# Kernel tuning notes

Hardware: AMD Instinct MI355X
Metric: run time of the kernel (lower is better)

## Reference

```python
import jax, jax.numpy as jnp
import numpy as np

N_NODES = 50000
N_EDGES = 300000
D = 256  # node/edge feature dim; MLP input = 3*D = 768


def setup_inputs() -> dict:
    key = jax.random.key(0)
    ks = jax.random.split(key, 5)
    x_node = jax.random.normal(ks[0], (N_NODES, D), dtype=jnp.float32)
    x_edge = jax.random.normal(ks[1], (N_EDGES, D), dtype=jnp.float32)
    edge_index = jax.random.randint(ks[2], (2, N_EDGES), 0, N_NODES, dtype=jnp.int64)
    # MLP params: Linear(3*D, D) -> ReLU -> Linear(D, D)
    W1 = jax.random.normal(ks[3], (3 * D, D), dtype=jnp.float32) * (1.0 / np.sqrt(3 * D))
    b1 = jnp.zeros((D,), dtype=jnp.float32)
    W2 = jax.random.normal(ks[4], (D, D), dtype=jnp.float32) * (1.0 / np.sqrt(D))
    b2 = jnp.zeros((D,), dtype=jnp.float32)
    return {"x_node": x_node, "x_edge": x_edge, "edge_index": edge_index,
            "W1": W1, "b1": b1, "W2": W2, "b2": b2}


def reference(x_node, x_edge, edge_index, W1, b1, W2, b2):
    # gather src/dst node feats and concat with edge feats: [E, 3*D]
    src = x_node[edge_index[0]]
    dst = x_node[edge_index[1]]
    h = jnp.concatenate([src, dst, x_edge], axis=1)
    # MLP (custom_func): Linear -> ReLU -> Linear
    h = jax.nn.relu(h @ W1 + b1)
    x_edge_ = h @ W2 + b2
    return x_edge_
```

## Files before the change

### kernel.cpp

```cpp
#include <hip/hip_runtime.h>


typedef __attribute__((ext_vector_type(8))) short short8;
typedef __attribute__((ext_vector_type(4))) float f32x4;

typedef __attribute__((address_space(1))) unsigned int* gp1_t;
typedef __attribute__((address_space(3))) unsigned int* lp3_t;

#define AS_OFF 0
#define BS_OFF 8192
#define HS_OFF 40960
#define SMEM_SZ 73728
#define LDO 260

__device__ __forceinline__ unsigned short f2b(float f) {
  unsigned int u = __float_as_uint(f);
  return (unsigned short)((u + 0x7FFFu + ((u >> 16) & 1u)) >> 16);
}
__device__ __forceinline__ unsigned int f2b2(float lo, float hi) {
  return (unsigned int)f2b(lo) | ((unsigned int)f2b(hi) << 16);
}
__device__ __forceinline__ void gload16(const void* g, void* l) {
  __builtin_amdgcn_global_load_lds((gp1_t)g, (lp3_t)l, 16, 0, 0);
}

__global__ void prep_w_kernel(const float* __restrict__ w,
                              unsigned short* __restrict__ wp, int total) {
  int i = blockIdx.x * 256 + threadIdx.x;
  if (i >= total) return;
  int kc = i >> 13;
  int rem = i & 8191;
  int n = rem >> 5;
  int kin = rem & 31;
  wp[i] = f2b(w[(size_t)(kc * 32 + kin) * 256 + n]);
}

__global__ void conv_bf16_kernel(const float* __restrict__ x,
                                 unsigned short* __restrict__ y, int n4) {
  int i = blockIdx.x * 256 + threadIdx.x;
  if (i >= n4) return;
  float4 v = ((const float4*)x)[i];
  ushort4 u;
  u.x = f2b(v.x); u.y = f2b(v.y); u.z = f2b(v.z); u.w = f2b(v.w);
  ((ushort4*)y)[i] = u;
}

__global__ __launch_bounds__(256, 2) void edge_mlp_kernel(
    const float* __restrict__ xnode, const float* __restrict__ xedge,
    const int* __restrict__ eidx,
    const unsigned short* __restrict__ nodeb, int use_nodeb,
    const unsigned short* __restrict__ wt1p, const float* __restrict__ b1,
    const unsigned short* __restrict__ wt2p, const float* __restrict__ b2,
    float* __restrict__ out, int E) {
  __shared__ __align__(16) char smem[SMEM_SZ];
  char* As = smem + AS_OFF;
  char* Bs = smem + BS_OFF;
  char* Hs = smem + HS_OFF;

  const int t = threadIdx.x;
  const int w = t >> 6, l = t & 63;
  const int lr = l & 15, lk = l >> 4;
  const int row4 = t >> 2;
  const int c4 = t & 3;

  const int ebase = blockIdx.x * 64;
  int e = ebase + row4;
  if (e >= E) e = E - 1;
  const int isrc = eidx[e], idst = eidx[E + e];

  f32x4 acc[4][4];
#pragma unroll
  for (int i = 0; i < 4; ++i)
#pragma unroll
    for (int j = 0; j < 4; ++j) acc[i][j] = (f32x4)0.0f;

  auto stageB = [&](const unsigned short* wp, int kc, int buf) {
    const char* g = (const char*)wp + (size_t)kc * 16384 + t * 16;
    char* lb = Bs + buf * 16384 + (w << 10);
#pragma unroll
    for (int q = 0; q < 4; ++q) gload16(g + q * 4096, lb + q * 4096);
  };
  auto stageA_node = [&](int kc, int buf) {
    const int node = (kc < 8) ? isrc : idst;
    const char* g = (const char*)nodeb + (size_t)node * 512 + (kc & 7) * 64 + c4 * 16;
    gload16(g, As + buf * 4096 + (w << 10));
  };
  auto stageA_load = [&](int kc, float4& m0, float4& m1) {
    const float* src;
    if (kc < 8)        src = xnode + (size_t)isrc * 256 + kc * 32 + c4 * 8;
    else if (kc < 16)  src = xnode + (size_t)idst * 256 + (kc - 8) * 32 + c4 * 8;
    else               src = xedge + (size_t)e * 256 + (kc - 16) * 32 + c4 * 8;
    m0 = *(const float4*)src;
    m1 = *(const float4*)(src + 4);
  };
  auto stageA_write = [&](int buf, float4 m0, float4 m1) {
    uint4 u;
    u.x = f2b2(m0.x, m0.y); u.y = f2b2(m0.z, m0.w);
    u.z = f2b2(m1.x, m1.y); u.w = f2b2(m1.z, m1.w);
    *(uint4*)(As + buf * 4096 + t * 16) = u;
  };

  auto compute1 = [&](int buf) {
    short8 af[4], bf[4];
    const char* ab = As + buf * 4096;
    const char* bb = Bs + buf * 16384;
#pragma unroll
    for (int mi = 0; mi < 4; ++mi)
      af[mi] = *(const short8*)(ab + (mi * 16 + lr) * 64 + lk * 16);
#pragma unroll
    for (int ni = 0; ni < 4; ++ni)
      bf[ni] = *(const short8*)(bb + (w * 64 + ni * 16 + lr) * 64 + lk * 16);
#pragma unroll
    for (int mi = 0; mi < 4; ++mi)
#pragma unroll
      for (int ni = 0; ni < 4; ++ni)
        acc[mi][ni] = __builtin_amdgcn_mfma_f32_16x16x32_bf16(
            af[mi], bf[ni], acc[mi][ni], 0, 0, 0);
  };

  stageB(wt1p, 0, 0);
  if (use_nodeb) {
    stageA_node(0, 0);
  } else {
    float4 a0, a1;
    stageA_load(0, a0, a1);
    stageA_write(0, a0, a1);
  }
  __syncthreads();

  for (int kc = 0; kc < 24; ++kc) {
    const int cur = kc & 1, nb = cur ^ 1;
    float4 m0, m1;
    bool man = false;
    if (kc < 23) {
      const int nk = kc + 1;
      stageB(wt1p, nk, nb);
      if (use_nodeb && nk < 16) {
        stageA_node(nk, nb);
      } else {
        stageA_load(nk, m0, m1);
        man = true;
      }
    } else {
      stageB(wt2p, 0, nb);
    }
    compute1(cur);
    if (man) stageA_write(nb, m0, m1);
    __syncthreads();
  }

#pragma unroll
  for (int ni = 0; ni < 4; ++ni) {
    const int col = w * 64 + ni * 16 + lr;
    const float bias = b1[col];
    const int cole = col & ~1;
    const int chunk = cole >> 3;
    const int cb = (cole & 6) * 2;
#pragma unroll
    for (int mi = 0; mi < 4; ++mi) {
      float v[4], p[4];
#pragma unroll
      for (int r = 0; r < 4; ++r) {
        float x = acc[mi][ni][r] + bias;
        v[r] = x > 0.f ? x : 0.f;
        acc[mi][ni][r] = 0.f;
      }
#pragma unroll
      for (int r = 0; r < 4; ++r) p[r] = __shfl_xor(v[r], 1, 64);
      const int r0 = (lr & 1) ? 2 : 0;
#pragma unroll
      for (int rr = 0; rr < 2; ++rr) {
        const int r = r0 + rr;
        const int row = mi * 16 + lk * 4 + r;
        const float lo = (lr & 1) ? p[r] : v[r];
        const float hi = (lr & 1) ? v[r] : p[r];
        *(unsigned int*)(Hs + row * 512 + ((chunk ^ (row & 7)) << 4) + cb) = f2b2(lo, hi);
      }
    }
  }
  __syncthreads();

  for (int kc2 = 0; kc2 < 8; ++kc2) {
    const int cur = kc2 & 1, nb = cur ^ 1;
    if (kc2 < 7) stageB(wt2p, kc2 + 1, nb);
    {
      short8 af[4], bf[4];
      const char* bb = Bs + cur * 16384;
#pragma unroll
      for (int mi = 0; mi < 4; ++mi) {
        const int row = mi * 16 + lr;
        af[mi] = *(const short8*)(Hs + row * 512 + (((kc2 * 4 + lk) ^ (row & 7)) << 4));
      }
#pragma unroll
      for (int ni = 0; ni < 4; ++ni)
        bf[ni] = *(const short8*)(bb + (w * 64 + ni * 16 + lr) * 64 + lk * 16);
#pragma unroll
      for (int mi = 0; mi < 4; ++mi)
#pragma unroll
        for (int ni = 0; ni < 4; ++ni)
          acc[mi][ni] = __builtin_amdgcn_mfma_f32_16x16x32_bf16(
              af[mi], bf[ni], acc[mi][ni], 0, 0, 0);
    }
    __syncthreads();
  }

  float* outst = (float*)smem;
#pragma unroll
  for (int ni = 0; ni < 4; ++ni) {
    const int col = w * 64 + ni * 16 + lr;
    const float bias = b2[col];
#pragma unroll
    for (int mi = 0; mi < 4; ++mi)
#pragma unroll
      for (int r = 0; r < 4; ++r)
        outst[(mi * 16 + lk * 4 + r) * LDO + col] = acc[mi][ni][r] + bias;
  }
  __syncthreads();
#pragma unroll
  for (int it = 0; it < 16; ++it) {
    const int idx = it * 1024 + t * 4;
    const int lrow = idx >> 8;
    const int cc = idx & 255;
    const int grow = ebase + lrow;
    if (grow < E)
      *(float4*)(out + (size_t)grow * 256 + cc) =
          *(const float4*)(outst + lrow * LDO + cc);
  }
}

extern "C" void kernel_launch(void* const* d_in, const int* in_sizes, int n_in,
                              void* d_out, int out_size, void* d_ws, size_t ws_size,
                              hipStream_t stream) {
  const float* xnode = (const float*)d_in[0];
  const float* xedge = (const float*)d_in[1];
  const int* eidx = (const int*)d_in[2];
  const float* W1 = (const float*)d_in[3];
  const float* b1 = (const float*)d_in[4];
  const float* W2 = (const float*)d_in[5];
  const float* b2 = (const float*)d_in[6];
  float* out = (float*)d_out;

  const int NN = in_sizes[0] / 256;
  const int E = in_sizes[1] / 256;

  char* ws = (char*)d_ws;
  unsigned short* wt1p = (unsigned short*)ws;
  unsigned short* wt2p = (unsigned short*)(ws + 24 * 16384);
  unsigned short* nodeb = (unsigned short*)(ws + 32 * 16384);
  const size_t need = (size_t)32 * 16384 + (size_t)NN * 512;
  const int use_nodeb = (ws_size >= need) ? 1 : 0;

  prep_w_kernel<<<(24 * 8192 + 255) / 256, 256, 0, stream>>>(W1, wt1p, 24 * 8192);
  prep_w_kernel<<<(8 * 8192 + 255) / 256, 256, 0, stream>>>(W2, wt2p, 8 * 8192);
  if (use_nodeb) {
    const int n4 = NN * 64;
    conv_bf16_kernel<<<(n4 + 255) / 256, 256, 0, stream>>>(xnode, nodeb, n4);
  }

  edge_mlp_kernel<<<(E + 63) / 64, 256, 0, stream>>>(
      xnode, xedge, eidx, nodeb, use_nodeb, wt1p, b1, wt2p, b2, out, E);
}
```

Before: 379.8 us.

## Enlarge edge tile to 256 rows with 512-thread blocks and swizzled LDS layout

The fused edge MLP kernel now processes 256 edges per block with 8 waves (2x4 wave grid, 128x64 per wave). It uses K-steps of 64, XOR-swizzled A/B tiles in 128 KB of LDS, and a reordered weight prepack that matches the swizzle. The second GEMM reads W2 fragments straight from global memory into registers with double buffering instead of staging them in LDS. The output is written back in four 64-row passes. The aim is more weight reuse per block and fewer LDS bank conflicts, at the cost of one block per CU and higher register pressure from 32 accumulators per thread.

Result: faster. 372.0 us (-2.1%).

```diff
diff --git a/kernel.cpp b/kernel.cpp
--- a/kernel.cpp
+++ b/kernel.cpp
@@ -3,14 +3,10 @@
 
 typedef __attribute__((ext_vector_type(8))) short short8;
 typedef __attribute__((ext_vector_type(4))) float f32x4;
-
 typedef __attribute__((address_space(1))) unsigned int* gp1_t;
 typedef __attribute__((address_space(3))) unsigned int* lp3_t;
 
-#define AS_OFF 0
-#define BS_OFF 8192
-#define HS_OFF 40960
-#define SMEM_SZ 73728
+#define SMEM_SZ 131072
 #define LDO 260
 
 __device__ __forceinline__ unsigned short f2b(float f) {
@@ -28,11 +24,13 @@
                               unsigned short* __restrict__ wp, int total) {
   int i = blockIdx.x * 256 + threadIdx.x;
   if (i >= total) return;
-  int kc = i >> 13;
-  int rem = i & 8191;
-  int n = rem >> 5;
-  int kin = rem & 31;
-  wp[i] = f2b(w[(size_t)(kc * 32 + kin) * 256 + n]);
+  int step = i >> 14;
+  int rem = i & 16383;
+  int n = rem >> 6;
+  int s = (rem >> 3) & 7;
+  int j = i & 7;
+  int k = step * 64 + (((s ^ (n & 7)) << 3) | j);
+  wp[i] = f2b(w[(size_t)k * 256 + n]);
 }
 
 __global__ void conv_bf16_kernel(const float* __restrict__ x,
@@ -45,7 +43,7 @@
   ((ushort4*)y)[i] = u;
 }
 
-__global__ __launch_bounds__(256, 2) void edge_mlp_kernel(
+__global__ __launch_bounds__(512) void edge_mlp_full(
     const float* __restrict__ xnode, const float* __restrict__ xedge,
     const int* __restrict__ eidx,
     const unsigned short* __restrict__ nodeb, int use_nodeb,
@@ -53,111 +51,125 @@
     const unsigned short* __restrict__ wt2p, const float* __restrict__ b2,
     float* __restrict__ out, int E) {
   __shared__ __align__(16) char smem[SMEM_SZ];
-  char* As = smem + AS_OFF;
-  char* Bs = smem + BS_OFF;
-  char* Hs = smem + HS_OFF;
-
-  const int t = threadIdx.x;
-  const int w = t >> 6, l = t & 63;
+
+  const int t = threadIdx.x, w = t >> 6, l = t & 63;
   const int lr = l & 15, lk = l >> 4;
-  const int row4 = t >> 2;
-  const int c4 = t & 3;
-
-  const int ebase = blockIdx.x * 64;
-  int e = ebase + row4;
-  if (e >= E) e = E - 1;
-  const int isrc = eidx[e], idst = eidx[E + e];
-
-  f32x4 acc[4][4];
-#pragma unroll
-  for (int i = 0; i < 4; ++i)
+  const int wr = w >> 2, wc = w & 3;
+  const int ebase = blockIdx.x * 256;
+
+  int nsrcq[4], ndstq[4];
+#pragma unroll
+  for (int q = 0; q < 4; ++q) {
+    int rq = 32 * w + 8 * q + (l >> 3);
+    int eq = ebase + rq;
+    if (eq >= E) eq = E - 1;
+    nsrcq[q] = eidx[eq];
+    ndstq[q] = eidx[E + eq];
+  }
+  const int swz16 = ((l & 7) ^ ((l >> 3) & 7)) << 4;
+  const int r2 = t >> 1;
+  int e2 = ebase + r2;
+  if (e2 >= E) e2 = E - 1;
+  const int ns2 = eidx[e2], nd2 = eidx[E + e2];
+
+  f32x4 acc[8][4];
+#pragma unroll
+  for (int i = 0; i < 8; ++i)
 #pragma unroll
     for (int j = 0; j < 4; ++j) acc[i][j] = (f32x4)0.0f;
 
-  auto stageB = [&](const unsigned short* wp, int kc, int buf) {
-    const char* g = (const char*)wp + (size_t)kc * 16384 + t * 16;
-    char* lb = Bs + buf * 16384 + (w << 10);
-#pragma unroll
-    for (int q = 0; q < 4; ++q) gload16(g + q * 4096, lb + q * 4096);
-  };
-  auto stageA_node = [&](int kc, int buf) {
-    const int node = (kc < 8) ? isrc : idst;
-    const char* g = (const char*)nodeb + (size_t)node * 512 + (kc & 7) * 64 + c4 * 16;
-    gload16(g, As + buf * 4096 + (w << 10));
-  };
-  auto stageA_load = [&](int kc, float4& m0, float4& m1) {
-    const float* src;
-    if (kc < 8)        src = xnode + (size_t)isrc * 256 + kc * 32 + c4 * 8;
-    else if (kc < 16)  src = xnode + (size_t)idst * 256 + (kc - 8) * 32 + c4 * 8;
-    else               src = xedge + (size_t)e * 256 + (kc - 16) * 32 + c4 * 8;
-    m0 = *(const float4*)src;
-    m1 = *(const float4*)(src + 4);
-  };
-  auto stageA_write = [&](int buf, float4 m0, float4 m1) {
-    uint4 u;
-    u.x = f2b2(m0.x, m0.y); u.y = f2b2(m0.z, m0.w);
-    u.z = f2b2(m1.x, m1.y); u.w = f2b2(m1.z, m1.w);
-    *(uint4*)(As + buf * 4096 + t * 16) = u;
-  };
-
-  auto compute1 = [&](int buf) {
-    short8 af[4], bf[4];
-    const char* ab = As + buf * 4096;
-    const char* bb = Bs + buf * 16384;
-#pragma unroll
-    for (int mi = 0; mi < 4; ++mi)
-      af[mi] = *(const short8*)(ab + (mi * 16 + lr) * 64 + lk * 16);
-#pragma unroll
-    for (int ni = 0; ni < 4; ++ni)
-      bf[ni] = *(const short8*)(bb + (w * 64 + ni * 16 + lr) * 64 + lk * 16);
-#pragma unroll
-    for (int mi = 0; mi < 4; ++mi)
-#pragma unroll
-      for (int ni = 0; ni < 4; ++ni)
-        acc[mi][ni] = __builtin_amdgcn_mfma_f32_16x16x32_bf16(
-            af[mi], bf[ni], acc[mi][ni], 0, 0, 0);
-  };
-
-  stageB(wt1p, 0, 0);
-  if (use_nodeb) {
-    stageA_node(0, 0);
-  } else {
-    float4 a0, a1;
-    stageA_load(0, a0, a1);
-    stageA_write(0, a0, a1);
-  }
+  auto stageB = [&](int step, int buf) {
+    const char* g = (const char*)wt1p + (size_t)step * 32768 + (t << 4);
+    char* d = smem + 65536 + buf * 32768 + (w << 10) + (l << 4);
+#pragma unroll
+    for (int q = 0; q < 4; ++q) gload16(g + q * 8192, d + q * 8192);
+  };
+  auto stageA_node = [&](int s, int buf) {
+    const int colb = (s & 3) * 128;
+    char* d = smem + buf * 32768 + (w << 12) + (l << 4);
+#pragma unroll
+    for (int q = 0; q < 4; ++q) {
+      const int nid = (s < 4) ? nsrcq[q] : ndstq[q];
+      gload16((const char*)nodeb + (size_t)nid * 512 + colb + swz16,
+              d + (q << 10));
+    }
+  };
+  auto stageA_f32 = [&](const float* base, int rowid, int coloff, int buf) {
+    const int rb = r2 & 7;
+    float4 v[8];
+#pragma unroll
+    for (int jj = 0; jj < 4; ++jj) {
+      const int j = (t & 1) * 4 + jj;
+      const float* p = base + (size_t)rowid * 256 + coloff + j * 8;
+      v[2 * jj] = ((const float4*)p)[0];
+      v[2 * jj + 1] = ((const float4*)p)[1];
+    }
+#pragma unroll
+    for (int jj = 0; jj < 4; ++jj) {
+      const int j = (t & 1) * 4 + jj;
+      uint4 u;
+      u.x = f2b2(v[2 * jj].x, v[2 * jj].y);
+      u.y = f2b2(v[2 * jj].z, v[2 * jj].w);
+      u.z = f2b2(v[2 * jj + 1].x, v[2 * jj + 1].y);
+      u.w = f2b2(v[2 * jj + 1].z, v[2 * jj + 1].w);
+      *(uint4*)(smem + buf * 32768 + r2 * 128 + ((j ^ rb) << 4)) = u;
+    }
+  };
+  auto stageA = [&](int s, int buf) {
+    if (s < 8) {
+      if (use_nodeb) stageA_node(s, buf);
+      else stageA_f32(xnode, (s < 4) ? ns2 : nd2, (s & 3) * 64, buf);
+    } else {
+      stageA_f32(xedge, e2, (s - 8) * 64, buf);
+    }
+  };
+  auto compute = [&](int k) {
+    const char* A = smem + (k & 1) * 32768;
+    const char* B = smem + 65536 + (k & 1) * 32768;
+    __builtin_amdgcn_s_setprio(1);
+#pragma unroll
+    for (int ks = 0; ks < 2; ++ks) {
+      short8 bf[4];
+#pragma unroll
+      for (int ni = 0; ni < 4; ++ni) {
+        const int n = wc * 64 + ni * 16 + lr;
+        bf[ni] = *(const short8*)(B + n * 128 + (((ks * 4 + lk) ^ (n & 7)) << 4));
+      }
+#pragma unroll
+      for (int mi = 0; mi < 8; ++mi) {
+        const int m = wr * 128 + mi * 16 + lr;
+        short8 af = *(const short8*)(A + m * 128 + (((ks * 4 + lk) ^ (m & 7)) << 4));
+#pragma unroll
+        for (int ni = 0; ni < 4; ++ni)
+          acc[mi][ni] = __builtin_amdgcn_mfma_f32_16x16x32_bf16(
+              af, bf[ni], acc[mi][ni], 0, 0, 0);
+      }
+    }
+    __builtin_amdgcn_s_setprio(0);
+  };
+
+  stageA(0, 0);
+  stageB(0, 0);
   __syncthreads();
-
-  for (int kc = 0; kc < 24; ++kc) {
-    const int cur = kc & 1, nb = cur ^ 1;
-    float4 m0, m1;
-    bool man = false;
-    if (kc < 23) {
-      const int nk = kc + 1;
-      stageB(wt1p, nk, nb);
-      if (use_nodeb && nk < 16) {
-        stageA_node(nk, nb);
-      } else {
-        stageA_load(nk, m0, m1);
-        man = true;
-      }
-    } else {
-      stageB(wt2p, 0, nb);
-    }
-    compute1(cur);
-    if (man) stageA_write(nb, m0, m1);
+  for (int k = 0; k < 12; ++k) {
+    if (k + 1 < 12) {
+      stageB(k + 1, (k + 1) & 1);
+      stageA(k + 1, (k + 1) & 1);
+    }
+    compute(k);
     __syncthreads();
   }
 
+  char* Hs = smem;
 #pragma unroll
   for (int ni = 0; ni < 4; ++ni) {
-    const int col = w * 64 + ni * 16 + lr;
+    const int col = wc * 64 + ni * 16 + lr;
     const float bias = b1[col];
     const int cole = col & ~1;
     const int chunk = cole >> 3;
     const int cb = (cole & 6) * 2;
 #pragma unroll
-    for (int mi = 0; mi < 4; ++mi) {
+    for (int mi = 0; mi < 8; ++mi) {
       float v[4], p[4];
 #pragma unroll
       for (int r = 0; r < 4; ++r) {
@@ -171,60 +183,78 @@
 #pragma unroll
       for (int rr = 0; rr < 2; ++rr) {
         const int r = r0 + rr;
-        const int row = mi * 16 + lk * 4 + r;
+        const int row = wr * 128 + mi * 16 + lk * 4 + r;
         const float lo = (lr & 1) ? p[r] : v[r];
         const float hi = (lr & 1) ? v[r] : p[r];
-        *(unsigned int*)(Hs + row * 512 + ((chunk ^ (row & 7)) << 4) + cb) = f2b2(lo, hi);
+        *(unsigned int*)(Hs + row * 512 + ((chunk ^ (row & 7)) << 4) + cb) =
+            f2b2(lo, hi);
       }
     }
   }
   __syncthreads();
 
-  for (int kc2 = 0; kc2 < 8; ++kc2) {
-    const int cur = kc2 & 1, nb = cur ^ 1;
-    if (kc2 < 7) stageB(wt2p, kc2 + 1, nb);
-    {
-      short8 af[4], bf[4];
-      const char* bb = Bs + cur * 16384;
-#pragma unroll
-      for (int mi = 0; mi < 4; ++mi) {
-        const int row = mi * 16 + lr;
-        af[mi] = *(const short8*)(Hs + row * 512 + (((kc2 * 4 + lk) ^ (row & 7)) << 4));
-      }
+  short8 bfA[4], bfB[4];
+  auto loadB2 = [&](int pair, short8 (&bf)[4]) {
+    const char* wb = (const char*)wt2p + (pair >> 1) * 32768;
+    const int ksl = (pair & 1) * 4 + lk;
+#pragma unroll
+    for (int ni = 0; ni < 4; ++ni) {
+      const int n = wc * 64 + ni * 16 + lr;
+      bf[ni] = *(const short8*)(wb + n * 128 + ((ksl ^ (n & 7)) << 4));
+    }
+  };
+  auto mfmaH = [&](int pair, short8 (&bf)[4]) {
+    const int j = (pair >> 1) * 8 + (pair & 1) * 4 + lk;
+    __builtin_amdgcn_s_setprio(1);
+#pragma unroll
+    for (int mi = 0; mi < 8; ++mi) {
+      const int m = wr * 128 + mi * 16 + lr;
+      short8 af = *(const short8*)(Hs + m * 512 + ((j ^ (m & 7)) << 4));
 #pragma unroll
       for (int ni = 0; ni < 4; ++ni)
-        bf[ni] = *(const short8*)(bb + (w * 64 + ni * 16 + lr) * 64 + lk * 16);
-#pragma unroll
-      for (int mi = 0; mi < 4; ++mi)
-#pragma unroll
-        for (int ni = 0; ni < 4; ++ni)
-          acc[mi][ni] = __builtin_amdgcn_mfma_f32_16x16x32_bf16(
-              af[mi], bf[ni], acc[mi][ni], 0, 0, 0);
-    }
+        acc[mi][ni] = __builtin_amdgcn_mfma_f32_16x16x32_bf16(
+            af, bf[ni], acc[mi][ni], 0, 0, 0);
+    }
+    __builtin_amdgcn_s_setprio(0);
+  };
+  loadB2(0, bfA);
+#pragma unroll
+  for (int pair = 0; pair < 8; pair += 2) {
+    if (pair + 1 < 8) loadB2(pair + 1, bfB);
+    mfmaH(pair, bfA);
+    if (pair + 2 < 8) loadB2(pair + 2, bfA);
+    if (pair + 1 < 8) mfmaH(pair + 1, bfB);
+  }
+
+  float* outst = (float*)smem;
+#pragma unroll
+  for (int p = 0; p < 4; ++p) {
     __syncthreads();
-  }
-
-  float* outst = (float*)smem;
-#pragma unroll
-  for (int ni = 0; ni < 4; ++ni) {
-    const int col = w * 64 + ni * 16 + lr;
-    const float bias = b2[col];
-#pragma unroll
-    for (int mi = 0; mi < 4; ++mi)
-#pragma unroll
-      for (int r = 0; r < 4; ++r)
-        outst[(mi * 16 + lk * 4 + r) * LDO + col] = acc[mi][ni][r] + bias;
-  }
-  __syncthreads();
-#pragma unroll
-  for (int it = 0; it < 16; ++it) {
-    const int idx = it * 1024 + t * 4;
-    const int lrow = idx >> 8;
-    const int cc = idx & 255;
-    const int grow = ebase + lrow;
-    if (grow < E)
-      *(float4*)(out + (size_t)grow * 256 + cc) =
-          *(const float4*)(outst + lrow * LDO + cc);
+    if (wr == (p >> 1)) {
+#pragma unroll
+      for (int ni = 0; ni < 4; ++ni) {
+        const int col = wc * 64 + ni * 16 + lr;
+        const float bias = b2[col];
+#pragma unroll
+        for (int mh = 0; mh < 4; ++mh) {
+          const int mi = (p & 1) * 4 + mh;
+#pragma unroll
+          for (int r = 0; r < 4; ++r)
+            outst[(mh * 16 + lk * 4 + r) * LDO + col] = acc[mi][ni][r] + bias;
+        }
+      }
+    }
+    __syncthreads();
+#pragma unroll
+    for (int it = 0; it < 8; ++it) {
+      const int idx = it * 2048 + t * 4;
+      const int lrow = idx >> 8;
+      const int cc = idx & 255;
+      const int grow = ebase + p * 64 + lrow;
+      if (grow < E)
+        *(float4*)(out + (size_t)grow * 256 + cc) =
+            *(const float4*)(outst + lrow * LDO + cc);
+    }
   }
 }
 
@@ -245,18 +275,21 @@
 
   char* ws = (char*)d_ws;
   unsigned short* wt1p = (unsigned short*)ws;
-  unsigned short* wt2p = (unsigned short*)(ws + 24 * 16384);
-  unsigned short* nodeb = (unsigned short*)(ws + 32 * 16384);
-  const size_t need = (size_t)32 * 16384 + (size_t)NN * 512;
-  const int use_nodeb = (ws_size >= need) ? 1 : 0;
-
-  prep_w_kernel<<<(24 * 8192 + 255) / 256, 256, 0, stream>>>(W1, wt1p, 24 * 8192);
-  prep_w_kernel<<<(8 * 8192 + 255) / 256, 256, 0, stream>>>(W2, wt2p, 8 * 8192);
+  unsigned short* wt2p = (unsigned short*)(ws + 12 * 32768);
+  unsigned short* nodeb = (unsigned short*)(ws + 16 * 32768);
+  const size_t need_tbl = (size_t)16 * 32768 + (size_t)NN * 512;
+  const int use_nodeb = (ws_size >= need_tbl) ? 1 : 0;
+
+  prep_w_kernel<<<(12 * 16384 + 255) / 256, 256, 0, stream>>>(W1, wt1p,
+                                                              12 * 16384);
+  prep_w_kernel<<<(4 * 16384 + 255) / 256, 256, 0, stream>>>(W2, wt2p,
+                                                             4 * 16384);
   if (use_nodeb) {
     const int n4 = NN * 64;
     conv_bf16_kernel<<<(n4 + 255) / 256, 256, 0, stream>>>(xnode, nodeb, n4);
   }
 
-  edge_mlp_kernel<<<(E + 63) / 64, 256, 0, stream>>>(
-      xnode, xedge, eidx, nodeb, use_nodeb, wt1p, b1, wt2p, b2, out, E);
-}
+  const int grid = (E + 255) / 256;
+  edge_mlp_full<<<grid, 512, 0, stream>>>(xnode, xedge, eidx, nodeb, use_nodeb,
+                                          wt1p, b1, wt2p, b2, out, E);
+}
```
